# Kernel tuning notes

Measured on AMD Instinct MI355X. Metric: run time of the kernel, lower is better.

The kernel has to match this reference:

```python
import jax, jax.numpy as jnp
import numpy as np

N = 50000      # nodes
E = 800000     # edges
H = 4          # heads (all layers)
D = 64         # per-head out dim (n_hidden == n_classes == 64)
IN = 256       # in_feats; also H*D so identity residual is valid
NEG_SLOPE = 0.2


def setup_inputs() -> dict:
    key = jax.random.key(0)
    ks = jax.random.split(key, 16)
    x = jax.random.normal(ks[0], (N, IN), dtype=jnp.float32)
    src = jax.random.randint(ks[1], (E,), 0, N, dtype=jnp.int32)
    dst = jax.random.randint(ks[2], (E,), 0, N, dtype=jnp.int32)
    inp = {"x": x, "src": src, "dst": dst}
    fan_ins = [IN, H * D, H * D]  # layer input widths
    for i, fin in enumerate(fan_ins):
        s = 1.0 / np.sqrt(fin)
        inp[f"W{i}"] = jax.random.normal(ks[3 + 4 * i], (fin, H * D), dtype=jnp.float32) * s
        inp[f"al{i}"] = jax.random.normal(ks[4 + 4 * i], (H, D), dtype=jnp.float32) * s
        inp[f"ar{i}"] = jax.random.normal(ks[5 + 4 * i], (H, D), dtype=jnp.float32) * s
        inp[f"b{i}"] = jnp.zeros((H * D,), dtype=jnp.float32)
    return inp


def _gat_layer(h, src, dst, W, al, ar, b, residual, activate):
    # project: [N, in] @ [in, H*D] -> [N, H, D]
    feat = (h @ W).reshape(-1, H, D)
    el = jnp.sum(feat * al, axis=-1)            # [N, H]
    er = jnp.sum(feat * ar, axis=-1)            # [N, H]
    e = jax.nn.leaky_relu(el[src] + er[dst], NEG_SLOPE)  # [E, H]
    # edge softmax per destination node (stable: subtract per-dst max)
    emax = jax.ops.segment_max(e, dst, num_segments=N)  # [N, H]
    e = jnp.exp(e - emax[dst])
    denom = jax.ops.segment_sum(e, dst, num_segments=N)  # [N, H]
    alpha = e / denom[dst]                               # [E, H]
    # message + scatter-aggregate: [E, H, D] summed into [N, H, D]
    out = jax.ops.segment_sum(alpha[:, :, None] * feat[src], dst, num_segments=N)
    if residual:
        out = out + h.reshape(-1, H, D)  # identity residual (in == H*D)
    out = out + b.reshape(1, H, D)
    if activate:
        out = jax.nn.elu(out)
    return out


def reference(x, src, dst, W0, al0, ar0, b0, W1, al1, ar1, b1, W2, al2, ar2, b2):
    h = _gat_layer(x, src, dst, W0, al0, ar0, b0, False, True).reshape(N, H * D)
    h = _gat_layer(h, src, dst, W1, al1, ar1, b1, True, True).reshape(N, H * D)
    h = _gat_layer(h, src, dst, W2, al2, ar2, b2, True, False).mean(axis=1)  # [N, D]
    return h
```

## Files before the change

### kernel.cpp

```cpp
#include <hip/hip_runtime.h>
#include <math.h>

#define N_NODES 50000
#define N_EDGES 800000
#define HD 256
#define NHEAD 4
#define DH 64
#define NPAD 50048

#define GEMM_BLKS 782
#define PACK_BLKS 96
#define HIST_BLKS 1563
#define NB 49

typedef short bf16x8 __attribute__((ext_vector_type(8)));
typedef float f32x4 __attribute__((ext_vector_type(4)));

__device__ __forceinline__ unsigned short f2bf(float f) {
    unsigned u = __float_as_uint(f);
    return (unsigned short)((u + 0x7fffu + ((u >> 16) & 1u)) >> 16);
}
__device__ __forceinline__ float bf2f(unsigned short h) {
    return __uint_as_float((unsigned)h << 16);
}
__device__ __forceinline__ int origk(int k) {
    return (k & ~63) | ((k & 3) * 16 + ((k >> 2) & 15));
}

__device__ __forceinline__ void mfma_tile(const unsigned short* Asl,
                                          const unsigned short* wbase,
                                          int lane, f32x4 acc[4][4]) {
#pragma unroll
    for (int kk = 0; kk < 8; kk++) {
        bf16x8 a[4], b[4];
#pragma unroll
        for (int m = 0; m < 4; m++) {
            int r = m * 16 + (lane & 15);
            int kb = kk * 32 + (lane >> 4) * 8;
            int byt = (r * 512 + kb * 2) ^ ((r & 7) << 4);
            a[m] = *(const bf16x8*)((const char*)Asl + byt);
        }
#pragma unroll
        for (int n = 0; n < 4; n++)
            b[n] = *(const bf16x8*)(wbase + ((size_t)(n * 8 + kk) * 64 + lane) * 8);
#pragma unroll
        for (int m = 0; m < 4; m++)
#pragma unroll
            for (int n = 0; n < 4; n++)
                acc[m][n] = __builtin_amdgcn_mfma_f32_16x16x32_bf16(a[m], b[n],
                                                                    acc[m][n], 0, 0, 0);
    }
}

__device__ __forceinline__ void epilogue_tile(f32x4 acc[4][4], int bm, int wv, int lane,
                                              const float* __restrict__ al,
                                              const float* __restrict__ ar,
                                              unsigned short* __restrict__ C,
                                              unsigned short* __restrict__ el,
                                              float* __restrict__ er, int M) {
    int rr = lane >> 4, cc = lane & 15;
    float alv[4], arv[4];
#pragma unroll
    for (int n = 0; n < 4; n++) {
        alv[n] = al[wv * 64 + n * 16 + cc];
        arv[n] = ar[wv * 64 + n * 16 + cc];
    }
    float vl[16], vr[16];
#pragma unroll
    for (int m = 0; m < 4; m++)
#pragma unroll
        for (int r = 0; r < 4; r++) {
            float ep = 0.f, rp = 0.f;
#pragma unroll
            for (int n = 0; n < 4; n++) {
                ep = fmaf(acc[m][n][r], alv[n], ep);
                rp = fmaf(acc[m][n][r], arv[n], rp);
            }
            vl[m * 4 + r] = ep;
            vr[m * 4 + r] = rp;
        }
    float l8[8], r8[8];
#pragma unroll
    for (int i = 0; i < 8; i++) {
        float xs = (cc & 1) ? vl[2 * i] : vl[2 * i + 1];
        float xk = (cc & 1) ? vl[2 * i + 1] : vl[2 * i];
        l8[i] = xk + __shfl_xor(xs, 1);
        float ys = (cc & 1) ? vr[2 * i] : vr[2 * i + 1];
        float yk = (cc & 1) ? vr[2 * i + 1] : vr[2 * i];
        r8[i] = yk + __shfl_xor(ys, 1);
    }
    float l4[4], r4[4];
#pragma unroll
    for (int i = 0; i < 4; i++) {
        float xs = (cc & 2) ? l8[2 * i] : l8[2 * i + 1];
        float xk = (cc & 2) ? l8[2 * i + 1] : l8[2 * i];
        l4[i] = xk + __shfl_xor(xs, 2);
        float ys = (cc & 2) ? r8[2 * i] : r8[2 * i + 1];
        float yk = (cc & 2) ? r8[2 * i + 1] : r8[2 * i];
        r4[i] = yk + __shfl_xor(ys, 2);
    }
    float l2[2], r2[2];
#pragma unroll
    for (int i = 0; i < 2; i++) {
        float xs = (cc & 4) ? l4[2 * i] : l4[2 * i + 1];
        float xk = (cc & 4) ? l4[2 * i + 1] : l4[2 * i];
        l2[i] = xk + __shfl_xor(xs, 4);
        float ys = (cc & 4) ? r4[2 * i] : r4[2 * i + 1];
        float yk = (cc & 4) ? r4[2 * i + 1] : r4[2 * i];
        r2[i] = yk + __shfl_xor(ys, 4);
    }
    {
        float xs = (cc & 8) ? l2[0] : l2[1];
        float xk = (cc & 8) ? l2[1] : l2[0];
        float lv = xk + __shfl_xor(xs, 8);
        float ys = (cc & 8) ? r2[0] : r2[1];
        float yk = (cc & 8) ? r2[1] : r2[0];
        float rv = yk + __shfl_xor(ys, 8);
        int row_e = bm + (cc >> 2) * 16 + rr * 4 + (cc & 3);
        if (row_e < M) {
            el[(size_t)row_e * NHEAD + wv] = f2bf(lv);
            er[(size_t)row_e * NHEAD + wv] = rv;
        }
    }
#pragma unroll
    for (int m = 0; m < 4; m++) {
#pragma unroll
        for (int r = 0; r < 4; r++) {
            int row = bm + m * 16 + rr * 4 + r;
            if (row < M) {
                unsigned short p4[4] = {f2bf(acc[m][0][r]), f2bf(acc[m][1][r]),
                                        f2bf(acc[m][2][r]), f2bf(acc[m][3][r])};
                *(ushort4*)(C + (size_t)row * 256 + wv * 64 + cc * 4) = *(ushort4*)p4;
            }
        }
    }
}

__global__ __launch_bounds__(256) void fused_ph_k(const float* __restrict__ W0,
                                                  const float* __restrict__ W1,
                                                  const float* __restrict__ W2,
                                                  unsigned short* __restrict__ Wp,
                                                  const int* __restrict__ dst,
                                                  int* __restrict__ deg) {
    int blk = blockIdx.x, tid = threadIdx.x, wv = tid >> 6, lane = tid & 63;
    if (blk < PACK_BLKS) {
        int tile = blk * 4 + wv;
        int L = tile >> 7, t = tile & 127;
        const float* W = L == 0 ? W0 : L == 1 ? W1 : W2;
        int nt = t >> 3, kt = t & 7;
        int col = nt * 16 + (lane & 15);
        int kb = kt * 32 + (lane >> 4) * 8;
        unsigned short v[8];
#pragma unroll
        for (int j = 0; j < 8; j++) {
            int k = kb + j;
            if (L > 0) k = origk(k);
            v[j] = f2bf(W[(size_t)k * 256 + col]);
        }
        *(bf16x8*)(Wp + ((size_t)(L * 128 + t) * 64 + lane) * 8) = *(bf16x8*)v;
    } else {
        int t = (blk - PACK_BLKS) * 256 + tid;
        int e = t * 2;
        int* mydeg = deg + (size_t)(tid & 3) * NPAD;
        if (e + 1 < N_EDGES) {
            int2 d2 = *(const int2*)(dst + e);
            atomicAdd(&mydeg[d2.x], 1);
            atomicAdd(&mydeg[d2.y], 1);
        } else if (e < N_EDGES) {
            atomicAdd(&mydeg[dst[e]], 1);
        }
    }
}

__global__ __launch_bounds__(256) void fused_gs_k(const float* __restrict__ A,
                                                  const unsigned short* __restrict__ Wp,
                                                  const float* __restrict__ al,
                                                  const float* __restrict__ ar,
                                                  unsigned short* __restrict__ C,
                                                  unsigned short* __restrict__ el,
                                                  float* __restrict__ er,
                                                  const int* __restrict__ deg,
                                                  int* __restrict__ rowptr,
                                                  int* __restrict__ bsum, int M) {
    __shared__ unsigned short Asl[64 * 256];
    __shared__ int wsum2[4];
    int blk = blockIdx.x, tid = threadIdx.x, wv = tid >> 6, lane = tid & 63;
    if (blk < GEMM_BLKS) {
        int bm = blk * 64;
#pragma unroll
        for (int i = 0; i < 8; i++) {
            int chunk = i * 256 + tid;
            int r = chunk >> 5, kc = (chunk & 31) * 8;
            float4 f0, f1;
            if (bm + r < M) {
                const float* p = A + (size_t)(bm + r) * 256 + kc;
                f0 = *(const float4*)p;
                f1 = *(const float4*)(p + 4);
            } else {
                f0 = f1 = make_float4(0.f, 0.f, 0.f, 0.f);
            }
            unsigned short tmp[8] = {f2bf(f0.x), f2bf(f0.y), f2bf(f0.z), f2bf(f0.w),
                                     f2bf(f1.x), f2bf(f1.y), f2bf(f1.z), f2bf(f1.w)};
            int b = (r * 512 + kc * 2) ^ ((r & 7) << 4);
            *(bf16x8*)((char*)Asl + b) = *(bf16x8*)tmp;
        }
        __syncthreads();
        const unsigned short* wbase = Wp + (size_t)(wv * 4) * 8 * 64 * 8;
        f32x4 acc[4][4] = {};
        mfma_tile(Asl, wbase, lane, acc);
        epilogue_tile(acc, bm, wv, lane, al, ar, C, el, er, M);
    } else {
        int sblk = blk - GEMM_BLKS;
        int i0 = sblk * 1024 + tid * 4;
        int v[4], p[4];
#pragma unroll
        for (int j = 0; j < 4; j++) {
            int i = i0 + j;
            v[j] = (i < N_NODES)
                       ? deg[i] + deg[i + NPAD] + deg[i + 2 * NPAD] + deg[i + 3 * NPAD]
                       : 0;
        }
        p[0] = v[0]; p[1] = p[0] + v[1]; p[2] = p[1] + v[2]; p[3] = p[2] + v[3];
        int tot = p[3];
        int sc = tot;
#pragma unroll
        for (int o = 1; o < 64; o <<= 1) {
            int t = __shfl_up(sc, o);
            if (lane >= o) sc += t;
        }
        if (lane == 63) wsum2[wv] = sc;
        __syncthreads();
        int woff = 0;
#pragma unroll
        for (int w = 0; w < 4; w++)
            if (w < wv) woff += wsum2[w];
        int excl = woff + sc - tot;
#pragma unroll
        for (int j = 0; j < 4; j++) {
            int i = i0 + j;
            if (i < N_NODES) rowptr[i + 1] = excl + p[j];
        }
        if (tid == 255) bsum[sblk] = excl + p[3];
    }
}

__global__ __launch_bounds__(1024) void scan3_k(int* __restrict__ rowptr,
                                                const int* __restrict__ bsum,
                                                int* __restrict__ cursor, int nb) {
    __shared__ int boff_s;
    int tid = threadIdx.x;
    if (tid < 64) {
        int v = (tid < nb) ? bsum[tid] : 0;
        int sc = v;
#pragma unroll
        for (int o = 1; o < 64; o <<= 1) {
            int t = __shfl_up(sc, o);
            if ((tid & 63) >= o) sc += t;
        }
        if (tid == (int)blockIdx.x) boff_s = sc - v;
    }
    __syncthreads();
    int off = boff_s;
    int i = blockIdx.x * 1024 + tid;
    if (blockIdx.x == 0 && tid == 0) { rowptr[0] = 0; cursor[0] = 0; }
    if (i < N_NODES) {
        int v = rowptr[i + 1] + off;
        rowptr[i + 1] = v;
        if (i + 1 < N_NODES) cursor[i + 1] = v;
    }
}

__global__ void scatter_k(const int* __restrict__ src, const int* __restrict__ dst,
                          int* __restrict__ cursor, int* __restrict__ csr_src) {
    int e = (blockIdx.x * 256 + threadIdx.x) * 2;
    if (e + 1 < N_EDGES) {
        int2 s2 = *(const int2*)(src + e);
        int2 d2 = *(const int2*)(dst + e);
        csr_src[atomicAdd(&cursor[d2.x], 1)] = s2.x;
        csr_src[atomicAdd(&cursor[d2.y], 1)] = s2.y;
    } else if (e < N_EDGES) {
        csr_src[atomicAdd(&cursor[dst[e]], 1)] = src[e];
    }
}

__global__ __launch_bounds__(256) void gemm2_k(const unsigned short* __restrict__ A,
                                               const unsigned short* __restrict__ Wp,
                                               const float* __restrict__ al,
                                               const float* __restrict__ ar,
                                               unsigned short* __restrict__ C,
                                               unsigned short* __restrict__ el,
                                               float* __restrict__ er, int M) {
    __shared__ unsigned short Asl[2][64 * 256];
    int tid = threadIdx.x, wv = tid >> 6, lane = tid & 63;
    int bm0 = blockIdx.x * 128, bm1 = bm0 + 64;
#pragma unroll
    for (int i = 0; i < 8; i++) {
        int chunk = i * 256 + tid;
        int r = chunk >> 5;
        int c16 = (chunk & 31) ^ (r & 7);
        int grow = bm0 + r; if (grow >= M) grow = M - 1;
        __builtin_amdgcn_global_load_lds(
            (const __attribute__((address_space(1))) unsigned int*)
                (A + (size_t)grow * 256 + c16 * 8),
            (__attribute__((address_space(3))) unsigned int*)
                ((char*)Asl[0] + (size_t)chunk * 16),
            16, 0, 0);
    }
#pragma unroll
    for (int i = 0; i < 8; i++) {
        int chunk = i * 256 + tid;
        int r = chunk >> 5;
        int c16 = (chunk & 31) ^ (r & 7);
        int grow = bm1 + r; if (grow >= M) grow = M - 1;
        __builtin_amdgcn_global_load_lds(
            (const __attribute__((address_space(1))) unsigned int*)
                (A + (size_t)grow * 256 + c16 * 8),
            (__attribute__((address_space(3))) unsigned int*)
                ((char*)Asl[1] + (size_t)chunk * 16),
            16, 0, 0);
    }
    asm volatile("s_waitcnt vmcnt(8)" ::: "memory");
    __builtin_amdgcn_sched_barrier(0);
    __builtin_amdgcn_s_barrier();
    const unsigned short* wbase = Wp + (size_t)(wv * 4) * 8 * 64 * 8;
    f32x4 acc[4][4] = {};
    mfma_tile(Asl[0], wbase, lane, acc);
    asm volatile("s_waitcnt vmcnt(0)" ::: "memory");
    __builtin_amdgcn_sched_barrier(0);
    __builtin_amdgcn_s_barrier();
    epilogue_tile(acc, bm0, wv, lane, al, ar, C, el, er, M);
    f32x4 acc2[4][4] = {};
    mfma_tile(Asl[1], wbase, lane, acc2);
    epilogue_tile(acc2, bm1, wv, lane, al, ar, C, el, er, M);
}

template <int MODE>
__global__ __launch_bounds__(256) void agg_k(const int* __restrict__ rowptr,
                                             const int* __restrict__ csr_src,
                                             const unsigned short* __restrict__ el,
                                             const float* __restrict__ er,
                                             const unsigned short* __restrict__ feat,
                                             const unsigned short* __restrict__ resid,
                                             const float* __restrict__ bias,
                                             float* __restrict__ out,
                                             unsigned short* __restrict__ hb) {
    __shared__ int   ws_s[4][64];
    __shared__ float ws_w[4][4][68];
    int wv = threadIdx.x >> 6, lane = threadIdx.x & 63;
    int node = blockIdx.x * 4 + wv;
    if (node >= N_NODES) return;
    int beg = rowptr[node], end = rowptr[node + 1];
    float4 er4 = *(const float4*)(er + (size_t)node * 4);
    float4 acc0 = make_float4(0.f, 0.f, 0.f, 0.f);
    float4 acc1 = make_float4(0.f, 0.f, 0.f, 0.f);
    float4 den = make_float4(0.f, 0.f, 0.f, 0.f);
    int h = lane >> 4;
    int l8 = lane * 8;
    const char* fb = (const char*)feat;
    for (int base = beg; base < end; base += 64) {
        int j = base + lane;
        int soff = 0;
        float4 w = make_float4(0.f, 0.f, 0.f, 0.f);
        if (j < end) {
            int s = csr_src[j];
            soff = s << 9;
            ushort4 l4u = *(const ushort4*)(el + (size_t)s * 4);
            float vx = bf2f(l4u.x) + er4.x; vx = vx > 0.f ? vx : 0.2f * vx;
            float vy = bf2f(l4u.y) + er4.y; vy = vy > 0.f ? vy : 0.2f * vy;
            float vz = bf2f(l4u.z) + er4.z; vz = vz > 0.f ? vz : 0.2f * vz;
            float vw = bf2f(l4u.w) + er4.w; vw = vw > 0.f ? vw : 0.2f * vw;
            w.x = expf(vx); w.y = expf(vy); w.z = expf(vz); w.w = expf(vw);
            den.x += w.x; den.y += w.y; den.z += w.z; den.w += w.w;
        }
        ws_s[wv][lane] = soff;
        ws_w[wv][0][lane] = w.x;
        ws_w[wv][1][lane] = w.y;
        ws_w[wv][2][lane] = w.z;
        ws_w[wv][3][lane] = w.w;
        __builtin_amdgcn_wave_barrier();
        int cnt = end - base; if (cnt > 64) cnt = 64;
        int cnt4 = (cnt + 3) & ~3;
        for (int k = 0; k < cnt4; k += 4) {
            int4   so = *(const int4*)&ws_s[wv][k];
            float4 w4 = *(const float4*)&ws_w[wv][h][k];
            ushort4 u0 = *(const ushort4*)(fb + (so.x + l8));
            ushort4 u1 = *(const ushort4*)(fb + (so.y + l8));
            ushort4 u2 = *(const ushort4*)(fb + (so.z + l8));
            ushort4 u3 = *(const ushort4*)(fb + (so.w + l8));
            acc0.x = fmaf(w4.x, bf2f(u0.x), acc0.x);
            acc0.y = fmaf(w4.x, bf2f(u0.y), acc0.y);
            acc0.z = fmaf(w4.x, bf2f(u0.z), acc0.z);
            acc0.w = fmaf(w4.x, bf2f(u0.w), acc0.w);
            acc1.x = fmaf(w4.y, bf2f(u1.x), acc1.x);
            acc1.y = fmaf(w4.y, bf2f(u1.y), acc1.y);
            acc1.z = fmaf(w4.y, bf2f(u1.z), acc1.z);
            acc1.w = fmaf(w4.y, bf2f(u1.w), acc1.w);
            acc0.x = fmaf(w4.z, bf2f(u2.x), acc0.x);
            acc0.y = fmaf(w4.z, bf2f(u2.y), acc0.y);
            acc0.z = fmaf(w4.z, bf2f(u2.z), acc0.z);
            acc0.w = fmaf(w4.z, bf2f(u2.w), acc0.w);
            acc1.x = fmaf(w4.w, bf2f(u3.x), acc1.x);
            acc1.y = fmaf(w4.w, bf2f(u3.y), acc1.y);
            acc1.z = fmaf(w4.w, bf2f(u3.z), acc1.z);
            acc1.w = fmaf(w4.w, bf2f(u3.w), acc1.w);
        }
        __builtin_amdgcn_wave_barrier();
    }
    float4 acc;
    acc.x = acc0.x + acc1.x; acc.y = acc0.y + acc1.y;
    acc.z = acc0.z + acc1.z; acc.w = acc0.w + acc1.w;
#pragma unroll
    for (int o = 1; o < 64; o <<= 1) {
        den.x += __shfl_xor(den.x, o);
        den.y += __shfl_xor(den.y, o);
        den.z += __shfl_xor(den.z, o);
        den.w += __shfl_xor(den.w, o);
    }
    float den_me = h == 0 ? den.x : h == 1 ? den.y : h == 2 ? den.z : den.w;
    float r = den_me > 0.f ? 1.f / den_me : 0.f;
    int cc = lane & 15;
    float4 b4;
    b4.x = bias[h * 64 + 0 * 16 + cc];
    b4.y = bias[h * 64 + 1 * 16 + cc];
    b4.z = bias[h * 64 + 2 * 16 + cc];
    b4.w = bias[h * 64 + 3 * 16 + cc];
    float4 o4;
    o4.x = acc.x * r + b4.x;
    o4.y = acc.y * r + b4.y;
    o4.z = acc.z * r + b4.z;
    o4.w = acc.w * r + b4.w;
    if (MODE >= 1) {
        ushort4 r4 = *(const ushort4*)(resid + (size_t)node * HD + lane * 4);
        o4.x += bf2f(r4.x); o4.y += bf2f(r4.y);
        o4.z += bf2f(r4.z); o4.w += bf2f(r4.w);
    }
    if (MODE <= 1) {
        o4.x = o4.x > 0.f ? o4.x : expm1f(o4.x);
        o4.y = o4.y > 0.f ? o4.y : expm1f(o4.y);
        o4.z = o4.z > 0.f ? o4.z : expm1f(o4.z);
        o4.w = o4.w > 0.f ? o4.w : expm1f(o4.w);
        ushort4 hv;
        hv.x = f2bf(o4.x); hv.y = f2bf(o4.y); hv.z = f2bf(o4.z); hv.w = f2bf(o4.w);
        *(ushort4*)(hb + (size_t)node * HD + lane * 4) = hv;
    } else {
        o4.x += __shfl_xor(o4.x, 16); o4.x += __shfl_xor(o4.x, 32);
        o4.y += __shfl_xor(o4.y, 16); o4.y += __shfl_xor(o4.y, 32);
        o4.z += __shfl_xor(o4.z, 16); o4.z += __shfl_xor(o4.z, 32);
        o4.w += __shfl_xor(o4.w, 16); o4.w += __shfl_xor(o4.w, 32);
        if (lane < 16) {
            float* po = out + (size_t)node * DH;
            po[0 * 16 + lane] = o4.x * 0.25f;
            po[1 * 16 + lane] = o4.y * 0.25f;
            po[2 * 16 + lane] = o4.z * 0.25f;
            po[3 * 16 + lane] = o4.w * 0.25f;
        }
    }
}

extern "C" void kernel_launch(void* const* d_in, const int* in_sizes, int n_in,
                              void* d_out, int out_size, void* d_ws, size_t ws_size,
                              hipStream_t stream) {
    const float* x   = (const float*)d_in[0];
    const int*   src = (const int*)d_in[1];
    const int*   dst = (const int*)d_in[2];
    const float* W[3]  = {(const float*)d_in[3], (const float*)d_in[7],  (const float*)d_in[11]};
    const float* al[3] = {(const float*)d_in[4], (const float*)d_in[8],  (const float*)d_in[12]};
    const float* ar[3] = {(const float*)d_in[5], (const float*)d_in[9],  (const float*)d_in[13]};
    const float* bb[3] = {(const float*)d_in[6], (const float*)d_in[10], (const float*)d_in[14]};

    size_t big = (size_t)N_NODES * HD;
    unsigned short* featb = (unsigned short*)d_ws;
    unsigned short* hb1 = featb + big;
    unsigned short* hb2 = hb1 + big;
    unsigned short* el = hb2 + big;
    float* er = (float*)(el + (size_t)NPAD * NHEAD);
    int* deg     = (int*)(er + (size_t)NPAD * NHEAD);
    int* rowptr  = deg + 4 * NPAD;
    int* cursor  = rowptr + NPAD;
    int* csr_src = cursor + NPAD;
    int* bsum    = csr_src + N_EDGES;
    unsigned short* Wp = (unsigned short*)(bsum + 64);

    hipMemsetAsync(deg, 0, (size_t)4 * NPAD * 4, stream);
    fused_ph_k<<<PACK_BLKS + HIST_BLKS, 256, 0, stream>>>(W[0], W[1], W[2], Wp, dst, deg);
    fused_gs_k<<<GEMM_BLKS + NB, 256, 0, stream>>>(x, Wp, al[0], ar[0], featb, el, er,
                                                   deg, rowptr, bsum, N_NODES);
    scan3_k<<<NB, 1024, 0, stream>>>(rowptr, bsum, cursor, NB);
    scatter_k<<<(N_EDGES / 2 + 255) / 256, 256, 0, stream>>>(src, dst, cursor, csr_src);

    int g2grid = (N_NODES + 127) / 128;
    int agrid = (N_NODES + 3) / 4;

    agg_k<0><<<agrid, 256, 0, stream>>>(rowptr, csr_src, el, er, featb,
                                        nullptr, bb[0], nullptr, hb1);
    gemm2_k<<<g2grid, 256, 0, stream>>>(hb1, Wp + (size_t)1 * 128 * 64 * 8,
                                        al[1], ar[1], featb, el, er, N_NODES);
    agg_k<1><<<agrid, 256, 0, stream>>>(rowptr, csr_src, el, er, featb,
                                        hb1, bb[1], nullptr, hb2);
    gemm2_k<<<g2grid, 256, 0, stream>>>(hb2, Wp + (size_t)2 * 128 * 64 * 8,
                                        al[2], ar[2], featb, el, er, N_NODES);
    agg_k<2><<<agrid, 256, 0, stream>>>(rowptr, csr_src, el, er, featb,
                                        hb2, bb[2], (float*)d_out, nullptr);
}
```

Baseline: 334.7 us.

## Record per-edge ranks in histogram to replace atomic scatter with fused placement

The degree histogram now keeps the atomicAdd return value as a per-edge rank, and a new scan kernel computes per-copy offsets into the four histogram replicas. CSR placement then needs no atomics and is computed as rowptr + copy offset + rank. That placement is fused into the layer-0 GEMM launch so it overlaps the projection, while the scan moves into its own kernel ahead of it. This removes the separate scatter kernel and its atomic contention, at the cost of an extra rank buffer write/read and moving the scan off the GEMM overlap.

Measured after the change: 296.9 us. 11.3% less time.

```diff
diff --git a/kernel.cpp b/kernel.cpp
--- a/kernel.cpp
+++ b/kernel.cpp
@@ -10,7 +10,7 @@
 
 #define GEMM_BLKS 782
 #define PACK_BLKS 96
-#define HIST_BLKS 1563
+#define EDGE_BLKS 1563
 #define NB 49
 
 typedef short bf16x8 __attribute__((ext_vector_type(8)));
@@ -141,7 +141,8 @@
                                                   const float* __restrict__ W2,
                                                   unsigned short* __restrict__ Wp,
                                                   const int* __restrict__ dst,
-                                                  int* __restrict__ deg) {
+                                                  int* __restrict__ deg,
+                                                  int* __restrict__ rank) {
     int blk = blockIdx.x, tid = threadIdx.x, wv = tid >> 6, lane = tid & 63;
     if (blk < PACK_BLKS) {
         int tile = blk * 4 + wv;
@@ -164,26 +165,96 @@
         int* mydeg = deg + (size_t)(tid & 3) * NPAD;
         if (e + 1 < N_EDGES) {
             int2 d2 = *(const int2*)(dst + e);
-            atomicAdd(&mydeg[d2.x], 1);
-            atomicAdd(&mydeg[d2.y], 1);
+            int r0 = atomicAdd(&mydeg[d2.x], 1);
+            int r1 = atomicAdd(&mydeg[d2.y], 1);
+            *(int2*)(rank + e) = make_int2(r0, r1);
         } else if (e < N_EDGES) {
-            atomicAdd(&mydeg[dst[e]], 1);
-        }
-    }
-}
-
-__global__ __launch_bounds__(256) void fused_gs_k(const float* __restrict__ A,
-                                                  const unsigned short* __restrict__ Wp,
-                                                  const float* __restrict__ al,
-                                                  const float* __restrict__ ar,
-                                                  unsigned short* __restrict__ C,
-                                                  unsigned short* __restrict__ el,
-                                                  float* __restrict__ er,
-                                                  const int* __restrict__ deg,
-                                                  int* __restrict__ rowptr,
-                                                  int* __restrict__ bsum, int M) {
+            rank[e] = atomicAdd(&mydeg[dst[e]], 1);
+        }
+    }
+}
+
+__global__ __launch_bounds__(256) void scan1_k(const int* __restrict__ deg,
+                                               int* __restrict__ rowptr,
+                                               int* __restrict__ bsum,
+                                               int* __restrict__ cpyoff) {
+    __shared__ int wsum2[4];
+    int tid = threadIdx.x, lane = tid & 63, wv = tid >> 6;
+    int i0 = blockIdx.x * 1024 + tid * 4;
+    int v[4], p[4];
+#pragma unroll
+    for (int j = 0; j < 4; j++) {
+        int i = i0 + j;
+        if (i < N_NODES) {
+            int c0 = deg[i], c1 = deg[i + NPAD];
+            int c2 = deg[i + 2 * NPAD], c3 = deg[i + 3 * NPAD];
+            v[j] = c0 + c1 + c2 + c3;
+            cpyoff[i] = 0;
+            cpyoff[i + NPAD] = c0;
+            cpyoff[i + 2 * NPAD] = c0 + c1;
+            cpyoff[i + 3 * NPAD] = c0 + c1 + c2;
+        } else {
+            v[j] = 0;
+        }
+    }
+    p[0] = v[0]; p[1] = p[0] + v[1]; p[2] = p[1] + v[2]; p[3] = p[2] + v[3];
+    int tot = p[3];
+    int sc = tot;
+#pragma unroll
+    for (int o = 1; o < 64; o <<= 1) {
+        int t = __shfl_up(sc, o);
+        if (lane >= o) sc += t;
+    }
+    if (lane == 63) wsum2[wv] = sc;
+    __syncthreads();
+    int woff = 0;
+#pragma unroll
+    for (int w = 0; w < 4; w++)
+        if (w < wv) woff += wsum2[w];
+    int excl = woff + sc - tot;
+#pragma unroll
+    for (int j = 0; j < 4; j++) {
+        int i = i0 + j;
+        if (i < N_NODES) rowptr[i + 1] = excl + p[j];
+    }
+    if (tid == 255) bsum[blockIdx.x] = excl + p[3];
+}
+
+__global__ __launch_bounds__(1024) void scan3_k(int* __restrict__ rowptr,
+                                                const int* __restrict__ bsum, int nb) {
+    __shared__ int boff_s;
+    int tid = threadIdx.x;
+    if (tid < 64) {
+        int v = (tid < nb) ? bsum[tid] : 0;
+        int sc = v;
+#pragma unroll
+        for (int o = 1; o < 64; o <<= 1) {
+            int t = __shfl_up(sc, o);
+            if ((tid & 63) >= o) sc += t;
+        }
+        if (tid == (int)blockIdx.x) boff_s = sc - v;
+    }
+    __syncthreads();
+    int off = boff_s;
+    int i = blockIdx.x * 1024 + tid;
+    if (blockIdx.x == 0 && tid == 0) rowptr[0] = 0;
+    if (i < N_NODES) rowptr[i + 1] += off;
+}
+
+__global__ __launch_bounds__(256) void fused_gsc_k(const float* __restrict__ A,
+                                                   const unsigned short* __restrict__ Wp,
+                                                   const float* __restrict__ al,
+                                                   const float* __restrict__ ar,
+                                                   unsigned short* __restrict__ C,
+                                                   unsigned short* __restrict__ el,
+                                                   float* __restrict__ er,
+                                                   const int* __restrict__ src,
+                                                   const int* __restrict__ dst,
+                                                   const int* __restrict__ rank,
+                                                   const int* __restrict__ rowptr,
+                                                   const int* __restrict__ cpyoff,
+                                                   int* __restrict__ csr_src, int M) {
     __shared__ unsigned short Asl[64 * 256];
-    __shared__ int wsum2[4];
     int blk = blockIdx.x, tid = threadIdx.x, wv = tid >> 6, lane = tid & 63;
     if (blk < GEMM_BLKS) {
         int bm = blk * 64;
@@ -210,76 +281,19 @@
         mfma_tile(Asl, wbase, lane, acc);
         epilogue_tile(acc, bm, wv, lane, al, ar, C, el, er, M);
     } else {
-        int sblk = blk - GEMM_BLKS;
-        int i0 = sblk * 1024 + tid * 4;
-        int v[4], p[4];
-#pragma unroll
-        for (int j = 0; j < 4; j++) {
-            int i = i0 + j;
-            v[j] = (i < N_NODES)
-                       ? deg[i] + deg[i + NPAD] + deg[i + 2 * NPAD] + deg[i + 3 * NPAD]
-                       : 0;
-        }
-        p[0] = v[0]; p[1] = p[0] + v[1]; p[2] = p[1] + v[2]; p[3] = p[2] + v[3];
-        int tot = p[3];
-        int sc = tot;
-#pragma unroll
-        for (int o = 1; o < 64; o <<= 1) {
-            int t = __shfl_up(sc, o);
-            if (lane >= o) sc += t;
-        }
-        if (lane == 63) wsum2[wv] = sc;
-        __syncthreads();
-        int woff = 0;
-#pragma unroll
-        for (int w = 0; w < 4; w++)
-            if (w < wv) woff += wsum2[w];
-        int excl = woff + sc - tot;
-#pragma unroll
-        for (int j = 0; j < 4; j++) {
-            int i = i0 + j;
-            if (i < N_NODES) rowptr[i + 1] = excl + p[j];
-        }
-        if (tid == 255) bsum[sblk] = excl + p[3];
-    }
-}
-
-__global__ __launch_bounds__(1024) void scan3_k(int* __restrict__ rowptr,
-                                                const int* __restrict__ bsum,
-                                                int* __restrict__ cursor, int nb) {
-    __shared__ int boff_s;
-    int tid = threadIdx.x;
-    if (tid < 64) {
-        int v = (tid < nb) ? bsum[tid] : 0;
-        int sc = v;
-#pragma unroll
-        for (int o = 1; o < 64; o <<= 1) {
-            int t = __shfl_up(sc, o);
-            if ((tid & 63) >= o) sc += t;
-        }
-        if (tid == (int)blockIdx.x) boff_s = sc - v;
-    }
-    __syncthreads();
-    int off = boff_s;
-    int i = blockIdx.x * 1024 + tid;
-    if (blockIdx.x == 0 && tid == 0) { rowptr[0] = 0; cursor[0] = 0; }
-    if (i < N_NODES) {
-        int v = rowptr[i + 1] + off;
-        rowptr[i + 1] = v;
-        if (i + 1 < N_NODES) cursor[i + 1] = v;
-    }
-}
-
-__global__ void scatter_k(const int* __restrict__ src, const int* __restrict__ dst,
-                          int* __restrict__ cursor, int* __restrict__ csr_src) {
-    int e = (blockIdx.x * 256 + threadIdx.x) * 2;
-    if (e + 1 < N_EDGES) {
-        int2 s2 = *(const int2*)(src + e);
-        int2 d2 = *(const int2*)(dst + e);
-        csr_src[atomicAdd(&cursor[d2.x], 1)] = s2.x;
-        csr_src[atomicAdd(&cursor[d2.y], 1)] = s2.y;
-    } else if (e < N_EDGES) {
-        csr_src[atomicAdd(&cursor[dst[e]], 1)] = src[e];
+        int t = (blk - GEMM_BLKS) * 256 + tid;
+        int e = t * 2;
+        const int* myoff = cpyoff + (size_t)(tid & 3) * NPAD;
+        if (e + 1 < N_EDGES) {
+            int2 s2 = *(const int2*)(src + e);
+            int2 d2 = *(const int2*)(dst + e);
+            int2 r2 = *(const int2*)(rank + e);
+            csr_src[rowptr[d2.x] + myoff[d2.x] + r2.x] = s2.x;
+            csr_src[rowptr[d2.y] + myoff[d2.y] + r2.y] = s2.y;
+        } else if (e < N_EDGES) {
+            int d = dst[e];
+            csr_src[rowptr[d] + myoff[d] + rank[e]] = src[e];
+        }
     }
 }
 
@@ -475,18 +489,21 @@
     unsigned short* el = hb2 + big;
     float* er = (float*)(el + (size_t)NPAD * NHEAD);
     int* deg     = (int*)(er + (size_t)NPAD * NHEAD);
-    int* rowptr  = deg + 4 * NPAD;
-    int* cursor  = rowptr + NPAD;
-    int* csr_src = cursor + NPAD;
+    int* cpyoff  = deg + 4 * NPAD;
+    int* rowptr  = cpyoff + 4 * NPAD;
+    int* rank    = rowptr + NPAD;
+    int* csr_src = rank + N_EDGES;
     int* bsum    = csr_src + N_EDGES;
     unsigned short* Wp = (unsigned short*)(bsum + 64);
 
     hipMemsetAsync(deg, 0, (size_t)4 * NPAD * 4, stream);
-    fused_ph_k<<<PACK_BLKS + HIST_BLKS, 256, 0, stream>>>(W[0], W[1], W[2], Wp, dst, deg);
-    fused_gs_k<<<GEMM_BLKS + NB, 256, 0, stream>>>(x, Wp, al[0], ar[0], featb, el, er,
-                                                   deg, rowptr, bsum, N_NODES);
-    scan3_k<<<NB, 1024, 0, stream>>>(rowptr, bsum, cursor, NB);
-    scatter_k<<<(N_EDGES / 2 + 255) / 256, 256, 0, stream>>>(src, dst, cursor, csr_src);
+    fused_ph_k<<<PACK_BLKS + EDGE_BLKS, 256, 0, stream>>>(W[0], W[1], W[2], Wp,
+                                                          dst, deg, rank);
+    scan1_k<<<NB, 256, 0, stream>>>(deg, rowptr, bsum, cpyoff);
+    scan3_k<<<NB, 1024, 0, stream>>>(rowptr, bsum, NB);
+    fused_gsc_k<<<GEMM_BLKS + EDGE_BLKS, 256, 0, stream>>>(
+        x, Wp, al[0], ar[0], featb, el, er, src, dst, rank, rowptr, cpyoff,
+        csr_src, N_NODES);
 
     int g2grid = (N_NODES + 127) / 128;
     int agrid = (N_NODES + 3) / 4;
```
